# Optimization experiments

Measured on AMD Instinct MI355X. Metric: run time of the kernel, lower is better.

## Reference

```python
import jax, jax.numpy as jnp
import numpy as np

B, T, C = 4, 2048, 2048
H = 16
D = C // H  # 128


def setup_inputs() -> dict:
    key = jax.random.key(0)
    ks = jax.random.split(key, 9)
    s = 0.02
    return {
        "x": jax.random.normal(ks[0], (B, T, C), dtype=jnp.float32),
        "wq": jax.random.normal(ks[1], (C, C), dtype=jnp.float32) * s,
        "bq": jax.random.normal(ks[2], (C,), dtype=jnp.float32) * s,
        "wk": jax.random.normal(ks[3], (C, C), dtype=jnp.float32) * s,
        "bk": jax.random.normal(ks[4], (C,), dtype=jnp.float32) * s,
        "wv": jax.random.normal(ks[5], (C, C), dtype=jnp.float32) * s,
        "bv": jax.random.normal(ks[6], (C,), dtype=jnp.float32) * s,
        "wo": jax.random.normal(ks[7], (C, C), dtype=jnp.float32) * s,
        "bo": jax.random.normal(ks[8], (C,), dtype=jnp.float32) * s,
    }


def reference(x, wq, bq, wk, bk, wv, bv, wo, bo):
    Bz, Tz, Cz = x.shape
    # projections (torch Linear: x @ W^T + b)
    q = (x @ wq.T + bq).reshape(Bz, Tz, H, D).transpose(0, 2, 1, 3)  # [B,H,T,D]
    k = (x @ wk.T + bk).reshape(Bz, Tz, H, D).transpose(0, 2, 1, 3)
    v = (x @ wv.T + bv).reshape(Bz, Tz, H, D).transpose(0, 2, 1, 3)
    scale = 1.0 / jnp.sqrt(jnp.float32(D))
    scores = jnp.einsum("bhqd,bhkd->bhqk", q, k) * scale  # [B,H,T,T]
    causal = jnp.tril(jnp.ones((Tz, Tz), dtype=bool))
    scores = jnp.where(causal, scores, jnp.float32(-jnp.inf))
    att = jax.nn.softmax(scores, axis=-1)
    out = jnp.einsum("bhqk,bhkd->bhqd", att, v)  # [B,H,T,D]
    out = out.transpose(0, 2, 1, 3).reshape(Bz, Tz, Cz)
    out = out @ wo.T + bo
    return out
```

## Files before the change

kernel.cpp:

```cpp
#include <hip/hip_runtime.h>
#include <hip/hip_bf16.h>

typedef float  f32x4  __attribute__((ext_vector_type(4)));
typedef __bf16 bf16x8 __attribute__((ext_vector_type(8)));
typedef __bf16 bf16x4 __attribute__((ext_vector_type(4)));

#define Bz 4
#define Tz 2048
#define Cz 2048
#define Hh 16
#define Dd 128
#define Mm 8192

__device__ __forceinline__ void gload_lds16(const __bf16* g, __bf16* l) {
  __builtin_amdgcn_global_load_lds(
      (const __attribute__((address_space(1))) void*)g,
      (__attribute__((address_space(3))) void*)l, 16, 0, 0);
}

__global__ __launch_bounds__(256)
void cvt_bf16(const float* __restrict__ in, __bf16* __restrict__ out, int n8) {
  int i = blockIdx.x * 256 + threadIdx.x;
  if (i >= n8) return;
  size_t base = (size_t)i * 8;
  f32x4 a = *(const f32x4*)(in + base);
  f32x4 b = *(const f32x4*)(in + base + 4);
  bf16x8 o;
  o[0]=(__bf16)a[0]; o[1]=(__bf16)a[1]; o[2]=(__bf16)a[2]; o[3]=(__bf16)a[3];
  o[4]=(__bf16)b[0]; o[5]=(__bf16)b[1]; o[6]=(__bf16)b[2]; o[7]=(__bf16)b[3];
  *(bf16x8*)(out + base) = o;
}

template<int MODE>
__global__ __launch_bounds__(256, 3)
void gemm_bt(const __bf16* __restrict__ A, const __bf16* __restrict__ W,
             const float* __restrict__ bias, void* __restrict__ Out,
             int K, float scale)
{
  __shared__ __bf16 As[128 * 64];
  __shared__ __bf16 Bs[128 * 64];

  const int tid  = threadIdx.x;
  const int lane = tid & 63;
  const int wave = tid >> 6;
  const int wm = wave >> 1, wn = wave & 1;
  const int g  = lane >> 4;
  const int lr = lane & 15;
  const int row0 = blockIdx.x * 128;
  const int col0 = blockIdx.y * 128;

  const int srow = lane >> 3;
  const int sblk = lane & 7;

  f32x4 acc[4][4] = {};

  for (int kt = 0; kt < K; kt += 64) {
    __syncthreads();
    #pragma unroll
    for (int p = 0; p < 4; ++p) {
      const int rb = p * 32 + wave * 8;
      const int r  = rb + srow;
      const int cb = sblk ^ (r & 7);
      gload_lds16(A + (size_t)(row0 + r) * K + kt + cb * 8, As + rb * 64);
      gload_lds16(W + (size_t)(col0 + r) * K + kt + cb * 8, Bs + rb * 64);
    }
    __syncthreads();
    #pragma unroll
    for (int kk = 0; kk < 2; ++kk) {
      bf16x8 af[4], bfr[4];
      #pragma unroll
      for (int i = 0; i < 4; ++i) {
        const int ar = wm * 64 + i * 16 + lr;
        af[i]  = *(const bf16x8*)(As + ar * 64 + ((((kk<<2)|g) ^ (ar & 7)) << 3));
        const int br = wn * 64 + i * 16 + lr;
        bfr[i] = *(const bf16x8*)(Bs + br * 64 + ((((kk<<2)|g) ^ (br & 7)) << 3));
      }
      #pragma unroll
      for (int i = 0; i < 4; ++i)
        #pragma unroll
        for (int j = 0; j < 4; ++j)
          acc[i][j] = __builtin_amdgcn_mfma_f32_16x16x32_bf16(af[i], bfr[j], acc[i][j], 0, 0, 0);
    }
  }

  #pragma unroll
  for (int j = 0; j < 4; ++j) {
    const int col = col0 + wn * 64 + j * 16 + lr;
    const float bv = bias[col];
    #pragma unroll
    for (int i = 0; i < 4; ++i) {
      if (MODE == 2) {
        const int row = row0 + wm * 64 + i * 16 + g * 4;
        const int b = row >> 11, t = row & (Tz - 1);
        const int h = col >> 7,  d = col & (Dd - 1);
        bf16x4 v4;
        #pragma unroll
        for (int r = 0; r < 4; ++r) v4[r] = (__bf16)(acc[i][j][r] + bv);
        *(bf16x4*)((__bf16*)Out + ((size_t)(b * Hh + h) * Dd + d) * Tz + t) = v4;
      } else {
        #pragma unroll
        for (int r = 0; r < 4; ++r) {
          const int row = row0 + wm * 64 + i * 16 + g * 4 + r;
          const float v = acc[i][j][r] + bv;
          if (MODE == 0) {
            const int b = row >> 11, t = row & (Tz - 1);
            const int h = col >> 7,  d = col & (Dd - 1);
            ((__bf16*)Out)[((size_t)(b * Hh + h) * Tz + t) * Dd + d] = (__bf16)(v * scale);
          } else {
            ((float*)Out)[(size_t)row * Cz + col] = v;
          }
        }
      }
    }
  }
}

__global__ __launch_bounds__(256, 2)
void attn_fwd(const __bf16* __restrict__ Q, const __bf16* __restrict__ Kg,
              const __bf16* __restrict__ Vt, __bf16* __restrict__ O)
{
  __shared__ __bf16 Ks[2][64 * 128];
  __shared__ __bf16 Vs[2][128 * 64];
  __shared__ __bf16 Ps[4][32 * 64];

  const int tid  = threadIdx.x;
  const int lane = tid & 63;
  const int wave = tid >> 6;
  const int g  = lane >> 4;
  const int lr = lane & 15;
  const int pair = blockIdx.x;
  const int bx   = blockIdx.y;
  const int b = pair >> 4, h = pair & 15;

  const __bf16* Qp = Q  + (size_t)pair * Tz * Dd;
  const __bf16* Kp = Kg + (size_t)pair * Tz * Dd;
  const __bf16* Vp = Vt + (size_t)pair * Dd * Tz;

  #define STAGE_KV(kv0_, buf_)                                                  \
    {                                                                           \
      const int kv0s = (kv0_);                                                  \
      _Pragma("unroll")                                                         \
      for (int p = 0; p < 4; ++p) {                                             \
        const int r  = p * 16 + wave * 4 + (lane >> 4);                         \
        const int cb = (lane & 15) ^ (r & 7);                                   \
        gload_lds16(Kp + (size_t)(kv0s + r) * Dd + cb * 8,                      \
                    &Ks[buf_][p * 2048 + wave * 512]);                          \
        const int d  = p * 32 + wave * 8 + (lane >> 3);                         \
        const int cv = (lane & 7) ^ (d & 7);                                    \
        gload_lds16(Vp + (size_t)d * Tz + kv0s + cv * 8,                        \
                    &Vs[buf_][p * 2048 + wave * 512]);                          \
      }                                                                         \
    }

  for (int pass = 0; pass < 2; ++pass) {
    const int qt  = pass == 0 ? (15 - bx) : bx;
    const int qw0 = qt * 128 + wave * 32;

    bf16x8 qf[2][4];
    #pragma unroll
    for (int im = 0; im < 2; ++im)
      #pragma unroll
      for (int ks = 0; ks < 4; ++ks)
        qf[im][ks] = *(const bf16x8*)(Qp + (size_t)(qw0 + im*16 + lr) * Dd + ks*32 + g*8);

    f32x4 oacc[2][8] = {};
    float mrow[2], lsum[2];
    mrow[0] = mrow[1] = -1e30f;
    lsum[0] = lsum[1] = 0.f;

    const int ntiles = 2 * qt + 2;

    STAGE_KV(0, 0);
    __syncthreads();

    for (int kt = 0; kt < ntiles; ++kt) {
      const int cur = kt & 1;
      const int kv0 = kt * 64;
      if (kt + 1 < ntiles) STAGE_KV((kt + 1) * 64, cur ^ 1);

      if (kv0 <= qw0 + 31) {
        f32x4 sacc[2][4] = {};
        __builtin_amdgcn_s_setprio(1);
        #pragma unroll
        for (int ks = 0; ks < 4; ++ks) {
          bf16x8 kf[4];
          #pragma unroll
          for (int in = 0; in < 4; ++in) {
            const int r = in*16 + lr;
            kf[in] = *(const bf16x8*)(&Ks[cur][r * 128 + ((((ks<<2)|g) ^ (r & 7)) << 3)]);
          }
          #pragma unroll
          for (int im = 0; im < 2; ++im)
            #pragma unroll
            for (int in = 0; in < 4; ++in)
              sacc[im][in] = __builtin_amdgcn_mfma_f32_16x16x32_bf16(kf[in], qf[im][ks], sacc[im][in], 0, 0, 0);
        }
        __builtin_amdgcn_s_setprio(0);

        if (kv0 + 63 > qw0) {
          #pragma unroll
          for (int im = 0; im < 2; ++im) {
            const int q = qw0 + im*16 + lr;
            #pragma unroll
            for (int in = 0; in < 4; ++in)
              #pragma unroll
              for (int r = 0; r < 4; ++r) {
                const int kv = kv0 + in*16 + g*4 + r;
                if (kv > q) sacc[im][in][r] = -3e38f;
              }
          }
        }

        #pragma unroll
        for (int im = 0; im < 2; ++im) {
          float m = fmaxf(fmaxf(sacc[im][0][0], sacc[im][0][1]),
                          fmaxf(sacc[im][0][2], sacc[im][0][3]));
          #pragma unroll
          for (int in = 1; in < 4; ++in)
            m = fmaxf(m, fmaxf(fmaxf(sacc[im][in][0], sacc[im][in][1]),
                               fmaxf(sacc[im][in][2], sacc[im][in][3])));
          m = fmaxf(m, __shfl_xor(m, 16));
          m = fmaxf(m, __shfl_xor(m, 32));

          const bool need = m > mrow[im] + 11.54f;
          if (__any(need)) {
            const float mn   = need ? m : mrow[im];
            const float corr = __builtin_amdgcn_exp2f(mrow[im] - mn);
            mrow[im] = mn;
            lsum[im] *= corr;
            const int sb = 20 * g;
            const float c0 = __shfl(corr, sb + 0);
            const float c1 = __shfl(corr, sb + 1);
            const float c2 = __shfl(corr, sb + 2);
            const float c3 = __shfl(corr, sb + 3);
            #pragma unroll
            for (int dn = 0; dn < 8; ++dn) {
              oacc[im][dn][0] *= c0; oacc[im][dn][1] *= c1;
              oacc[im][dn][2] *= c2; oacc[im][dn][3] *= c3;
            }
          }

          float rs = 0.f;
          const int prow = im*16 + lr;
          #pragma unroll
          for (int in = 0; in < 4; ++in) {
            const float p0 = __builtin_amdgcn_exp2f(sacc[im][in][0] - mrow[im]);
            const float p1 = __builtin_amdgcn_exp2f(sacc[im][in][1] - mrow[im]);
            const float p2 = __builtin_amdgcn_exp2f(sacc[im][in][2] - mrow[im]);
            const float p3 = __builtin_amdgcn_exp2f(sacc[im][in][3] - mrow[im]);
            rs += (p0 + p1) + (p2 + p3);
            bf16x4 q4;
            q4[0] = (__bf16)p0; q4[1] = (__bf16)p1;
            q4[2] = (__bf16)p2; q4[3] = (__bf16)p3;
            const int bs = (in*4 + g) ^ ((prow & 3) << 2);
            *(bf16x4*)(&Ps[wave][prow * 64 + bs * 4]) = q4;
          }
          rs += __shfl_xor(rs, 16);
          rs += __shfl_xor(rs, 32);
          lsum[im] += rs;
        }

        __builtin_amdgcn_s_setprio(1);
        #pragma unroll
        for (int kk = 0; kk < 2; ++kk) {
          bf16x8 pa[2];
          #pragma unroll
          for (int im = 0; im < 2; ++im) {
            const int prow = im*16 + lr;
            const int bs = (kk*8 + 2*g) ^ ((prow & 3) << 2);
            pa[im] = *(const bf16x8*)(&Ps[wave][prow * 64 + bs * 4]);
          }
          #pragma unroll
          for (int dn = 0; dn < 8; ++dn) {
            const int d = dn*16 + lr;
            bf16x8 vb = *(const bf16x8*)(&Vs[cur][d * 64 + ((((kk<<2)|g) ^ (d & 7)) << 3)]);
            #pragma unroll
            for (int im = 0; im < 2; ++im)
              oacc[im][dn] = __builtin_amdgcn_mfma_f32_16x16x32_bf16(pa[im], vb, oacc[im][dn], 0, 0, 0);
          }
        }
        __builtin_amdgcn_s_setprio(0);
      }
      __syncthreads();
    }

    #pragma unroll
    for (int im = 0; im < 2; ++im) {
      const float inv = 1.0f / lsum[im];
      const int sb = 20 * g;
      const float i0 = __shfl(inv, sb + 0);
      const float i1 = __shfl(inv, sb + 1);
      const float i2 = __shfl(inv, sb + 2);
      const float i3 = __shfl(inv, sb + 3);
      #pragma unroll
      for (int dn = 0; dn < 8; ++dn) {
        const int qrow = qw0 + im*16 + g*4;
        const int d    = h * Dd + dn*16 + lr;
        O[((size_t)(b * Tz + qrow + 0)) * Cz + d] = (__bf16)(oacc[im][dn][0] * i0);
        O[((size_t)(b * Tz + qrow + 1)) * Cz + d] = (__bf16)(oacc[im][dn][1] * i1);
        O[((size_t)(b * Tz + qrow + 2)) * Cz + d] = (__bf16)(oacc[im][dn][2] * i2);
        O[((size_t)(b * Tz + qrow + 3)) * Cz + d] = (__bf16)(oacc[im][dn][3] * i3);
      }
    }
  }
  #undef STAGE_KV
}

extern "C" void kernel_launch(void* const* d_in, const int* in_sizes, int n_in,
                              void* d_out, int out_size, void* d_ws, size_t ws_size,
                              hipStream_t stream) {
  const float* x  = (const float*)d_in[0];
  const float* wq = (const float*)d_in[1];
  const float* bq = (const float*)d_in[2];
  const float* wk = (const float*)d_in[3];
  const float* bk = (const float*)d_in[4];
  const float* wv = (const float*)d_in[5];
  const float* bv = (const float*)d_in[6];
  const float* wo = (const float*)d_in[7];
  const float* bo = (const float*)d_in[8];
  float* out = (float*)d_out;

  char* w = (char*)d_ws;
  __bf16* xb   = (__bf16*)w; w += (size_t)Mm * Cz * 2;
  __bf16* wbuf = (__bf16*)w; w += (size_t)Cz * Cz * 2;
  __bf16* qb   = (__bf16*)w; w += (size_t)Mm * Cz * 2;
  __bf16* kb   = (__bf16*)w; w += (size_t)Mm * Cz * 2;
  __bf16* vbuf = (__bf16*)w; w += (size_t)Mm * Cz * 2;
  if (ws_size < (size_t)(w - (char*)d_ws)) return;

  const int nx8 = Mm * Cz / 8;
  const int nw8 = Cz * Cz / 8;
  dim3 ggrid(Mm / 128, Cz / 128);
  const float qscale = 0.12752551286084110f;

  cvt_bf16<<<nx8 / 256, 256, 0, stream>>>(x, xb, nx8);

  cvt_bf16<<<nw8 / 256, 256, 0, stream>>>(wq, wbuf, nw8);
  gemm_bt<0><<<ggrid, 256, 0, stream>>>(xb, wbuf, bq, qb, Cz, qscale);

  cvt_bf16<<<nw8 / 256, 256, 0, stream>>>(wk, wbuf, nw8);
  gemm_bt<0><<<ggrid, 256, 0, stream>>>(xb, wbuf, bk, kb, Cz, 1.0f);

  cvt_bf16<<<nw8 / 256, 256, 0, stream>>>(wv, wbuf, nw8);
  gemm_bt<2><<<ggrid, 256, 0, stream>>>(xb, wbuf, bv, vbuf, Cz, 1.0f);

  __bf16* ob = xb;
  attn_fwd<<<dim3(Bz * Hh, 8), 256, 0, stream>>>(qb, kb, vbuf, ob);

  cvt_bf16<<<nw8 / 256, 256, 0, stream>>>(wo, wbuf, nw8);
  gemm_bt<1><<<ggrid, 256, 0, stream>>>(ob, wbuf, bo, out, Cz, 1.0f);
}
```

Baseline: 400.3 us.

## Fuse Q/K/V projections into one GEMM and batch weight conversions

Converts all four weight matrices to bf16 in a single launch, storing the concatenated QKV weight temporarily in the output buffer. The three separate projection GEMMs become one launch with a 48-column-tile grid that selects bias, scale and output layout per tile. This cuts kernel launches and the tail effect of three small grids, and gives more blocks per launch for occupancy. It reuses d_out as scratch, which works only because the final GEMM overwrites it afterwards.

```diff
diff --git a/kernel.cpp b/kernel.cpp
--- a/kernel.cpp
+++ b/kernel.cpp
@@ -31,11 +31,31 @@
   *(bf16x8*)(out + base) = o;
 }
 
-template<int MODE>
+__global__ __launch_bounds__(256)
+void cvt_w4(const float* __restrict__ w0, const float* __restrict__ w1,
+            const float* __restrict__ w2, const float* __restrict__ w3,
+            __bf16* __restrict__ wqkv, __bf16* __restrict__ wob) {
+  const int n8 = Cz * Cz / 8;
+  int i = blockIdx.x * 256 + threadIdx.x;
+  if (i >= n8) return;
+  const int which = blockIdx.y;
+  const float* src = which == 0 ? w0 : which == 1 ? w1 : which == 2 ? w2 : w3;
+  __bf16* dst = which == 3 ? wob : wqkv + (size_t)which * Cz * Cz;
+  size_t base = (size_t)i * 8;
+  f32x4 a = *(const f32x4*)(src + base);
+  f32x4 b = *(const f32x4*)(src + base + 4);
+  bf16x8 o;
+  o[0]=(__bf16)a[0]; o[1]=(__bf16)a[1]; o[2]=(__bf16)a[2]; o[3]=(__bf16)a[3];
+  o[4]=(__bf16)b[0]; o[5]=(__bf16)b[1]; o[6]=(__bf16)b[2]; o[7]=(__bf16)b[3];
+  *(bf16x8*)(dst + base) = o;
+}
+
 __global__ __launch_bounds__(256, 3)
-void gemm_bt(const __bf16* __restrict__ A, const __bf16* __restrict__ W,
-             const float* __restrict__ bias, void* __restrict__ Out,
-             int K, float scale)
+void gemm_qkv(const __bf16* __restrict__ A, const __bf16* __restrict__ W,
+              const float* __restrict__ bq, const float* __restrict__ bk,
+              const float* __restrict__ bv,
+              __bf16* __restrict__ qb, __bf16* __restrict__ kb,
+              __bf16* __restrict__ vb, float qscale)
 {
   __shared__ __bf16 As[128 * 64];
   __shared__ __bf16 Bs[128 * 64];
@@ -54,15 +74,15 @@
 
   f32x4 acc[4][4] = {};
 
-  for (int kt = 0; kt < K; kt += 64) {
+  for (int kt = 0; kt < Cz; kt += 64) {
     __syncthreads();
     #pragma unroll
     for (int p = 0; p < 4; ++p) {
       const int rb = p * 32 + wave * 8;
       const int r  = rb + srow;
       const int cb = sblk ^ (r & 7);
-      gload_lds16(A + (size_t)(row0 + r) * K + kt + cb * 8, As + rb * 64);
-      gload_lds16(W + (size_t)(col0 + r) * K + kt + cb * 8, Bs + rb * 64);
+      gload_lds16(A + (size_t)(row0 + r) * Cz + kt + cb * 8, As + rb * 64);
+      gload_lds16(W + (size_t)(col0 + r) * Cz + kt + cb * 8, Bs + rb * 64);
     }
     __syncthreads();
     #pragma unroll
@@ -83,35 +103,100 @@
     }
   }
 
+  const int seg  = col0 >> 11;
+  const int csg0 = col0 & 2047;
+  const float* bias = seg == 0 ? bq : (seg == 1 ? bk : bv);
+  const float scl   = seg == 0 ? qscale : 1.0f;
+  __bf16* outp      = seg == 0 ? qb : (seg == 1 ? kb : vb);
+
   #pragma unroll
   for (int j = 0; j < 4; ++j) {
-    const int col = col0 + wn * 64 + j * 16 + lr;
-    const float bv = bias[col];
+    const int col = csg0 + wn * 64 + j * 16 + lr;
+    const float bvv = bias[col];
     #pragma unroll
     for (int i = 0; i < 4; ++i) {
-      if (MODE == 2) {
+      if (seg == 2) {
         const int row = row0 + wm * 64 + i * 16 + g * 4;
         const int b = row >> 11, t = row & (Tz - 1);
         const int h = col >> 7,  d = col & (Dd - 1);
         bf16x4 v4;
         #pragma unroll
-        for (int r = 0; r < 4; ++r) v4[r] = (__bf16)(acc[i][j][r] + bv);
-        *(bf16x4*)((__bf16*)Out + ((size_t)(b * Hh + h) * Dd + d) * Tz + t) = v4;
+        for (int r = 0; r < 4; ++r) v4[r] = (__bf16)(acc[i][j][r] + bvv);
+        *(bf16x4*)(outp + ((size_t)(b * Hh + h) * Dd + d) * Tz + t) = v4;
       } else {
         #pragma unroll
         for (int r = 0; r < 4; ++r) {
           const int row = row0 + wm * 64 + i * 16 + g * 4 + r;
-          const float v = acc[i][j][r] + bv;
-          if (MODE == 0) {
-            const int b = row >> 11, t = row & (Tz - 1);
-            const int h = col >> 7,  d = col & (Dd - 1);
-            ((__bf16*)Out)[((size_t)(b * Hh + h) * Tz + t) * Dd + d] = (__bf16)(v * scale);
-          } else {
-            ((float*)Out)[(size_t)row * Cz + col] = v;
-          }
+          const int b = row >> 11, t = row & (Tz - 1);
+          const int h = col >> 7,  d = col & (Dd - 1);
+          outp[((size_t)(b * Hh + h) * Tz + t) * Dd + d] = (__bf16)((acc[i][j][r] + bvv) * scl);
         }
       }
     }
+  }
+}
+
+__global__ __launch_bounds__(256, 3)
+void gemm_o(const __bf16* __restrict__ A, const __bf16* __restrict__ W,
+            const float* __restrict__ bias, float* __restrict__ Out)
+{
+  __shared__ __bf16 As[128 * 64];
+  __shared__ __bf16 Bs[128 * 64];
+
+  const int tid  = threadIdx.x;
+  const int lane = tid & 63;
+  const int wave = tid >> 6;
+  const int wm = wave >> 1, wn = wave & 1;
+  const int g  = lane >> 4;
+  const int lr = lane & 15;
+  const int row0 = blockIdx.x * 128;
+  const int col0 = blockIdx.y * 128;
+
+  const int srow = lane >> 3;
+  const int sblk = lane & 7;
+
+  f32x4 acc[4][4] = {};
+
+  for (int kt = 0; kt < Cz; kt += 64) {
+    __syncthreads();
+    #pragma unroll
+    for (int p = 0; p < 4; ++p) {
+      const int rb = p * 32 + wave * 8;
+      const int r  = rb + srow;
+      const int cb = sblk ^ (r & 7);
+      gload_lds16(A + (size_t)(row0 + r) * Cz + kt + cb * 8, As + rb * 64);
+      gload_lds16(W + (size_t)(col0 + r) * Cz + kt + cb * 8, Bs + rb * 64);
+    }
+    __syncthreads();
+    #pragma unroll
+    for (int kk = 0; kk < 2; ++kk) {
+      bf16x8 af[4], bfr[4];
+      #pragma unroll
+      for (int i = 0; i < 4; ++i) {
+        const int ar = wm * 64 + i * 16 + lr;
+        af[i]  = *(const bf16x8*)(As + ar * 64 + ((((kk<<2)|g) ^ (ar & 7)) << 3));
+        const int br = wn * 64 + i * 16 + lr;
+        bfr[i] = *(const bf16x8*)(Bs + br * 64 + ((((kk<<2)|g) ^ (br & 7)) << 3));
+      }
+      #pragma unroll
+      for (int i = 0; i < 4; ++i)
+        #pragma unroll
+        for (int j = 0; j < 4; ++j)
+          acc[i][j] = __builtin_amdgcn_mfma_f32_16x16x32_bf16(af[i], bfr[j], acc[i][j], 0, 0, 0);
+    }
+  }
+
+  #pragma unroll
+  for (int j = 0; j < 4; ++j) {
+    const int col = col0 + wn * 64 + j * 16 + lr;
+    const float bvv = bias[col];
+    #pragma unroll
+    for (int i = 0; i < 4; ++i)
+      #pragma unroll
+      for (int r = 0; r < 4; ++r) {
+        const int row = row0 + wm * 64 + i * 16 + g * 4 + r;
+        Out[(size_t)row * Cz + col] = acc[i][j][r] + bvv;
+      }
   }
 }
 
@@ -322,31 +407,26 @@
 
   char* w = (char*)d_ws;
   __bf16* xb   = (__bf16*)w; w += (size_t)Mm * Cz * 2;
-  __bf16* wbuf = (__bf16*)w; w += (size_t)Cz * Cz * 2;
+  __bf16* wob  = (__bf16*)w; w += (size_t)Cz * Cz * 2;
   __bf16* qb   = (__bf16*)w; w += (size_t)Mm * Cz * 2;
   __bf16* kb   = (__bf16*)w; w += (size_t)Mm * Cz * 2;
   __bf16* vbuf = (__bf16*)w; w += (size_t)Mm * Cz * 2;
   if (ws_size < (size_t)(w - (char*)d_ws)) return;
 
+  __bf16* wqkv = (__bf16*)d_out;
+
   const int nx8 = Mm * Cz / 8;
   const int nw8 = Cz * Cz / 8;
-  dim3 ggrid(Mm / 128, Cz / 128);
   const float qscale = 0.12752551286084110f;
 
   cvt_bf16<<<nx8 / 256, 256, 0, stream>>>(x, xb, nx8);
-
-  cvt_bf16<<<nw8 / 256, 256, 0, stream>>>(wq, wbuf, nw8);
-  gemm_bt<0><<<ggrid, 256, 0, stream>>>(xb, wbuf, bq, qb, Cz, qscale);
-
-  cvt_bf16<<<nw8 / 256, 256, 0, stream>>>(wk, wbuf, nw8);
-  gemm_bt<0><<<ggrid, 256, 0, stream>>>(xb, wbuf, bk, kb, Cz, 1.0f);
-
-  cvt_bf16<<<nw8 / 256, 256, 0, stream>>>(wv, wbuf, nw8);
-  gemm_bt<2><<<ggrid, 256, 0, stream>>>(xb, wbuf, bv, vbuf, Cz, 1.0f);
+  cvt_w4<<<dim3(nw8 / 256, 4), 256, 0, stream>>>(wq, wk, wv, wo, wqkv, wob);
+
+  gemm_qkv<<<dim3(Mm / 128, 48), 256, 0, stream>>>(xb, wqkv, bq, bk, bv,
+                                                   qb, kb, vbuf, qscale);
 
   __bf16* ob = xb;
   attn_fwd<<<dim3(Bz * Hh, 8), 256, 0, stream>>>(qb, kb, vbuf, ob);
 
-  cvt_bf16<<<nw8 / 256, 256, 0, stream>>>(wo, wbuf, nw8);
-  gemm_bt<1><<<ggrid, 256, 0, stream>>>(ob, wbuf, bo, out, Cz, 1.0f);
-}
+  gemm_o<<<dim3(Mm / 128, Cz / 128), 256, 0, stream>>>(ob, wob, bo, out);
+}
```

New measurement: 385.5 us. 3.7% less time.
